# Kernel tuning notes

Measured on AMD Instinct MI355X. Metric: run time of the kernel, lower is better.

The kernel has to match this reference:

```python
import jax, jax.numpy as jnp
import numpy as np
import math

SEQ_LEN = 1024
NUM_FILTERS = 24
INPUT_DIM = 256
OUTPUT_DIM = 256
BATCH = 4


def _spectral_filters(seq_len, K):
    # Hankel matrix Z[i,j] = 2 / ((i+j)^3 - (i+j)), i,j in 1..L (use_hankel_L=False)
    entries = np.arange(1, seq_len + 1, dtype=np.float64)
    ipj = entries[:, None] + entries[None, :]
    Z = 2.0 / (ipj ** 3 - ipj)
    sigma, phi = np.linalg.eigh(Z)
    phi_k = phi[:, -K:] * (sigma[-K:] ** 0.25)
    return jnp.asarray(phi_k, dtype=jnp.float32)  # [L, K]


def setup_inputs() -> dict:
    key = jax.random.key(0)
    k1, k2, k3 = jax.random.split(key, 3)
    scale = (NUM_FILTERS * INPUT_DIM) ** (-0.5)
    x = jax.random.normal(k1, (BATCH, SEQ_LEN, INPUT_DIM), dtype=jnp.float32)
    phi = _spectral_filters(SEQ_LEN, NUM_FILTERS)
    M_phi_plus = jax.random.normal(k2, (NUM_FILTERS, INPUT_DIM, OUTPUT_DIM), dtype=jnp.float32) * scale
    M_phi_minus = jax.random.normal(k3, (NUM_FILTERS, INPUT_DIM, OUTPUT_DIM), dtype=jnp.float32) * scale
    return {"x": x, "phi": phi, "M_phi_plus": M_phi_plus, "M_phi_minus": M_phi_minus}


def reference(x, phi, M_phi_plus, M_phi_minus):
    B, L, I = x.shape
    n = 1 << math.ceil(math.log2(2 * L - 1))  # FFT length (2048 for L=1024)
    # alternating sign: +1 at even positions, -1 at odd (sgn[:,1::2] *= -1)
    sgn = jnp.where(jnp.arange(L) % 2 == 1, -1.0, 1.0).astype(jnp.float32)
    # FFT of filters: [F, K]
    V = jnp.fft.rfft(phi.astype(jnp.float32), n=n, axis=0)
    # FFT of input and sign-modulated input: [B, F, I]
    X = jnp.fft.rfft(x, n=n, axis=1)
    Xs = jnp.fft.rfft(x * sgn[None, :, None], n=n, axis=1)
    # pointwise multiply in frequency, broadcast over K: [B, F, K, I]
    U_plus = jnp.fft.irfft(V[None, :, :, None] * X[:, :, None, :], n=n, axis=1)[:, :L]
    U_minus = jnp.fft.irfft(V[None, :, :, None] * Xs[:, :, None, :], n=n, axis=1)[:, :L]
    U_minus = U_minus * sgn[None, :, None, None]
    # spectral projection: [B, L, O]
    out = jnp.einsum('blki,kio->blo', U_plus, M_phi_plus)
    out = out + jnp.einsum('blki,kio->blo', U_minus, M_phi_minus)
    return out
```

## Files before the change

### kernel.cpp

```cpp
#include <hip/hip_runtime.h>


#define ZB_ 12582912

typedef __attribute__((ext_vector_type(8))) short bf16x8;
typedef __attribute__((ext_vector_type(4))) float f32x4;

__device__ inline unsigned short f2bf(float f) {
    unsigned u = __float_as_uint(f);
    u += 0x7FFFu + ((u >> 16) & 1u);
    return (unsigned short)(u >> 16);
}

__device__ inline void gl16(const unsigned short* g, unsigned short* l) {
    __builtin_amdgcn_global_load_lds((const __attribute__((address_space(1))) void*)g,
                                     (__attribute__((address_space(3))) void*)l, 16, 0, 0);
}

__global__ __launch_bounds__(256) void k_prep_all(const float* __restrict__ x,
                                                  const float* __restrict__ phi,
                                                  const float* __restrict__ Mp,
                                                  const float* __restrict__ Mm,
                                                  unsigned short* __restrict__ xb,
                                                  unsigned short* __restrict__ ToepA,
                                                  unsigned short* __restrict__ MbT) {
    __shared__ float tile[32][33];
    int bid = blockIdx.x, tid = threadIdx.x;
    if (bid < 1024) {
        int i = (bid * 256 + tid) * 4;
        float4 v = *(const float4*)(x + i);
        ushort4 o;
        o.x = f2bf(v.x); o.y = f2bf(v.y); o.z = f2bf(v.z); o.w = f2bf(v.w);
        int row = i >> 8, col = i & 255;
        int dst = (row << 8) | (col & 192) | ((col & 63) ^ ((row & 7) << 3));
        *(ushort4*)(xb + dst) = o;
    } else if (bid < 1792) {
        int r = bid - 1024;
        int kk = r >> 4;
        int dm = (r & 15) - 1;
        int k = (kk < 24) ? kk : kk - 24;
        int i = tid >> 1, j0 = (tid & 1) * 32;
        unsigned short* dst = ToepA + ((size_t)kk * 16 + (dm + 1)) * 8192 + i * 64;
        int sw = (i & 7) << 3;
#pragma unroll
        for (int q = 0; q < 8; ++q) {
            int j = j0 + q * 4;
            unsigned short e[4];
#pragma unroll
            for (int ee = 0; ee < 4; ++ee) {
                int t = dm * 64 + i - (j + ee);
                float v = 0.f;
                if (t >= 0 && t < 1024) {
                    v = phi[t * 24 + k];
                    if (kk >= 24 && (t & 1)) v = -v;
                }
                e[ee] = f2bf(v);
            }
            ushort4 ov; ov.x = e[0]; ov.y = e[1]; ov.z = e[2]; ov.w = e[3];
            *(ushort4*)(dst + (j ^ sw)) = ov;
        }
    } else {
        int flat = bid - 1792;
        int kk = flat >> 6, rr = flat & 63;
        int i0 = (rr >> 3) * 32, o0 = (rr & 7) * 32;
        int tx = tid & 31, ty = tid >> 5;
        const float* src = ((kk < 24) ? Mp : Mm) + (size_t)((kk < 24) ? kk : kk - 24) * 65536;
        for (int j = 0; j < 4; ++j)
            tile[ty + j * 8][tx] = src[(i0 + ty + j * 8) * 256 + o0 + tx];
        __syncthreads();
        for (int j = 0; j < 4; ++j) {
            int orow = o0 + ty + j * 8, i = i0 + tx;
            int ic = (i & 192) | ((i & 63) ^ ((orow & 7) << 3));
            MbT[(size_t)kk * 65536 + orow * 256 + ic] = f2bf(tile[tx][ty + j * 8]);
        }
    }
}

__global__ __launch_bounds__(256, 2) void k_stage1(const unsigned short* __restrict__ xb0,
                                                   const unsigned short* __restrict__ MbT,
                                                   unsigned short* __restrict__ Z) {
    __shared__ unsigned short Ab[2][8192];
    __shared__ unsigned short Bb[3][8192];
    int tid = threadIdx.x, lane = tid & 63, w = tid >> 6;
    int wm = w >> 1, wn = w & 1;
    int m0 = blockIdx.x * 128;
    int kk = blockIdx.y >> 1;
    int o0 = (blockIdx.y & 1) * 128;
    int b  = blockIdx.z;
    const unsigned short* xb_b = xb0 + (size_t)b * 262144;
    unsigned short* Zb = Z + (size_t)b * ZB_;
    const unsigned short* Bsrc = MbT + (size_t)kk * 65536;
    int l16 = lane & 15, kofs = (lane >> 4) * 8;
    int sw = (l16 & 7) << 3;
    int r8 = lane >> 3, cg = lane & 7;

    int arow[4], brow[4], lofs[4];
#pragma unroll
    for (int q = 0; q < 4; ++q) {
        int rr = q * 32 + w * 8 + r8;
        arow[q] = (m0 + rr) * 256 + cg * 8;
        brow[q] = (o0 + rr) * 256 + cg * 8;
        lofs[q] = q * 2048 + w * 512;
    }

    f32x4 acc[4][4];
    for (int i = 0; i < 4; ++i)
        for (int j = 0; j < 4; ++j) {
            acc[i][j][0] = 0.f; acc[i][j][1] = 0.f; acc[i][j][2] = 0.f; acc[i][j][3] = 0.f;
        }

    auto stageA = [&](int bi, int ko) {
#pragma unroll
        for (int q = 0; q < 4; ++q) gl16(xb_b + arow[q] + ko * 64, &Ab[bi][0] + lofs[q]);
    };
    auto stageB = [&](int bi, int ko) {
#pragma unroll
        for (int q = 0; q < 4; ++q) gl16(Bsrc + brow[q] + ko * 64, &Bb[bi][0] + lofs[q]);
    };

    stageA(0, 0); stageB(0, 0); stageB(1, 1);

    for (int ko = 0; ko < 4; ++ko) {
        if (ko < 3) { asm volatile("s_waitcnt vmcnt(4)" ::: "memory"); }
        else        { asm volatile("s_waitcnt vmcnt(0)" ::: "memory"); }
        __builtin_amdgcn_sched_barrier(0);
        __builtin_amdgcn_s_barrier();
        __builtin_amdgcn_sched_barrier(0);
        if (ko < 3) stageA((ko + 1) & 1, ko + 1);
        if (ko < 2) stageB((ko + 2) % 3, ko + 2);

        const unsigned short* Abase = &Ab[ko & 1][0];
        const unsigned short* Bbase = &Bb[ko % 3][0];
        __builtin_amdgcn_s_setprio(1);
#pragma unroll
        for (int ks = 0; ks < 2; ++ks) {
            int koX = (ks * 32 + kofs) ^ sw;
            bf16x8 af[4], bfv[4];
#pragma unroll
            for (int mi = 0; mi < 4; ++mi)
                af[mi] = *(const bf16x8*)(Abase + (wm * 64 + mi * 16 + l16) * 64 + koX);
#pragma unroll
            for (int ni = 0; ni < 4; ++ni)
                bfv[ni] = *(const bf16x8*)(Bbase + (wn * 64 + ni * 16 + l16) * 64 + koX);
#pragma unroll
            for (int mi = 0; mi < 4; ++mi)
#pragma unroll
                for (int ni = 0; ni < 4; ++ni)
                    acc[mi][ni] = __builtin_amdgcn_mfma_f32_16x16x32_bf16(af[mi], bfv[ni], acc[mi][ni], 0, 0, 0);
        }
        __builtin_amdgcn_s_setprio(0);
    }

    int r4 = (lane >> 4) * 4;
    for (int mi = 0; mi < 4; ++mi) {
        int sbase = m0 + wm * 64 + mi * 16 + r4;
        for (int ni = 0; ni < 4; ++ni) {
            int o = o0 + wn * 64 + ni * 16 + l16;
            ushort4 pk;
            pk.x = f2bf(acc[mi][ni][0]); pk.y = f2bf(acc[mi][ni][1]);
            pk.z = f2bf(acc[mi][ni][2]); pk.w = f2bf(acc[mi][ni][3]);
            *(ushort4*)(Zb + (size_t)kk * 262144 + (size_t)o * 1024 + (sbase ^ ((o & 7) << 3))) = pk;
        }
    }
}

__global__ __launch_bounds__(256, 2) void k_stage2(const unsigned short* __restrict__ Z,
                                                   const unsigned short* __restrict__ ToepA,
                                                   float* __restrict__ partial, int kkpg) {
    __shared__ unsigned short Abuf[2][8192];
    __shared__ unsigned short Zbuf[3][8192];
    int tid = threadIdx.x, lane = tid & 63, w = tid >> 6;
    int wm = w >> 1, wn = w & 1;

    int gy = gridDim.y, nwg = 4 * gy * gridDim.z;
    int orig = blockIdx.x + blockIdx.y * 4 + blockIdx.z * 4 * gy;
    int wg = (orig & 7) * (nwg >> 3) + (orig >> 3);
    int pr = wg & 3;
    int yy = (wg >> 2) % gy;
    int zz = (wg >> 2) / gy;
    int o0 = (yy & 1) * 128;
    int b  = yy >> 1;
    int kgi = zz;
    int kk0 = kgi * kkpg;

    int l16 = lane & 15, kofs = (lane >> 4) * 8;
    int sw = (l16 & 7) << 3;
    int r8 = lane >> 3, cg = lane & 7;

    const unsigned short* Zb = Z + (size_t)b * ZB_;
    float* pb = partial + ((size_t)b * gridDim.z + kgi) * 262144;

    int arow[4], zrow[4], lofs[4];
#pragma unroll
    for (int q = 0; q < 4; ++q) {
        int rr = q * 32 + w * 8 + r8;
        arow[q] = rr * 64 + cg * 8;
        zrow[q] = (o0 + rr) * 1024 + cg * 8;
        lofs[q] = q * 2048 + w * 512;
    }

    for (int half = 0; half < 2; ++half) {
        int lb = half ? (7 - pr) : pr;
        int l0 = lb * 128;
        int nch = 2 * lb + 2;
        int total = kkpg * nch;

        f32x4 acc[4][4];
        for (int i = 0; i < 4; ++i)
            for (int j = 0; j < 4; ++j) {
                acc[i][j][0] = 0.f; acc[i][j][1] = 0.f; acc[i][j][2] = 0.f; acc[i][j][3] = 0.f;
            }

        __syncthreads();

        auto stageA = [&](int bi, int kka, int didx) {
            const unsigned short* gA = ToepA + ((size_t)kka * 16 + didx) * 8192;
#pragma unroll
            for (int q = 0; q < 4; ++q) gl16(gA + arow[q], &Abuf[bi][0] + lofs[q]);
        };
        auto stageZ = [&](int bi, int kka, int s0) {
            const unsigned short* gZ = Zb + (size_t)kka * 262144 + s0;
#pragma unroll
            for (int q = 0; q < 4; ++q) gl16(gZ + zrow[q], &Zbuf[bi][0] + lofs[q]);
        };
        auto compute = [&](int ba, int bz) {
            const unsigned short* Abase = &Abuf[ba][0];
            const unsigned short* Zbase = &Zbuf[bz][0];
            __builtin_amdgcn_s_setprio(1);
#pragma unroll
            for (int ks = 0; ks < 2; ++ks) {
                int koX = (ks * 32 + kofs) ^ sw;
                bf16x8 af[4], bfv[4];
#pragma unroll
                for (int mi = 0; mi < 4; ++mi)
                    af[mi] = *(const bf16x8*)(Abase + (wm * 64 + mi * 16 + l16) * 64 + koX);
#pragma unroll
                for (int ni = 0; ni < 4; ++ni)
                    bfv[ni] = *(const bf16x8*)(Zbase + (wn * 64 + ni * 16 + l16) * 64 + koX);
#pragma unroll
                for (int mi = 0; mi < 4; ++mi)
#pragma unroll
                    for (int ni = 0; ni < 4; ++ni)
                        acc[mi][ni] = __builtin_amdgcn_mfma_f32_16x16x32_bf16(af[mi], bfv[ni], acc[mi][ni], 0, 0, 0);
            }
            __builtin_amdgcn_s_setprio(0);
        };

        stageA(0, kk0, 2 * lb + 1);
        stageZ(0, kk0, 0);
        stageZ(1, kk0, 64);

        int scA = 1, kkA = 0;
        int scZ = 2, kkZ = 0;
        if (scZ == nch) { scZ = 0; kkZ = 1; }
        int jz = 2;

        for (int j = 0; j < total - 1; ++j) {
            asm volatile("s_waitcnt vmcnt(4)" ::: "memory");
            __builtin_amdgcn_sched_barrier(0);
            __builtin_amdgcn_s_barrier();
            __builtin_amdgcn_sched_barrier(0);
            stageA((j + 1) & 1, kk0 + kkA, 2 * lb - scA + 1);
            ++scA; if (scA == nch) { scA = 0; ++kkA; }
            if (jz < total) {
                stageZ(jz % 3, kk0 + kkZ, scZ * 64);
                ++scZ; if (scZ == nch) { scZ = 0; ++kkZ; }
                ++jz;
            }
            compute(j & 1, j % 3);
        }
        asm volatile("s_waitcnt vmcnt(0)" ::: "memory");
        __builtin_amdgcn_sched_barrier(0);
        __builtin_amdgcn_s_barrier();
        __builtin_amdgcn_sched_barrier(0);
        compute((total - 1) & 1, (total - 1) % 3);

        int r4 = (lane >> 4) * 4;
        for (int mi = 0; mi < 4; ++mi) {
            int l = l0 + wm * 64 + mi * 16 + r4;
            for (int ni = 0; ni < 4; ++ni) {
                int o = o0 + wn * 64 + ni * 16 + l16;
                float* dst = pb + (size_t)l * 256 + o;
                dst[0]   = acc[mi][ni][0];
                dst[256] = acc[mi][ni][1];
                dst[512] = acc[mi][ni][2];
                dst[768] = acc[mi][ni][3];
            }
        }
    }
}

__global__ void k_reduce(const float* __restrict__ partial, float* __restrict__ outg, int kg) {
    const float* pb = partial + (size_t)blockIdx.y * kg * 262144;
    int i = (blockIdx.x * 256 + threadIdx.x) * 4;
    float4 s = *(const float4*)(pb + i);
    for (int kgi = 1; kgi < kg; ++kgi) {
        float4 v = *(const float4*)(pb + (size_t)kgi * 262144 + i);
        s.x += v.x; s.y += v.y; s.z += v.z; s.w += v.w;
    }
    *(float4*)(outg + (size_t)blockIdx.y * 262144 + i) = s;
}

extern "C" void kernel_launch(void* const* d_in, const int* in_sizes, int n_in,
                              void* d_out, int out_size, void* d_ws, size_t ws_size,
                              hipStream_t stream) {
    const float* x   = (const float*)d_in[0];
    const float* phi = (const float*)d_in[1];
    const float* Mp  = (const float*)d_in[2];
    const float* Mm  = (const float*)d_in[3];
    float* out = (float*)d_out;

    char* ws = (char*)d_ws;
    unsigned short* xb    = (unsigned short*)(ws);
    unsigned short* MbT   = (unsigned short*)(ws + 2097152);
    unsigned short* ToepA = (unsigned short*)(ws + 8388608);
    unsigned short* Zbuf  = (unsigned short*)(ws + 20971520);
    const size_t fixed = 20971520;

    int g = 4, kg = 16;
    auto need = [&](int gg, int kk) {
        return fixed + (size_t)gg * 25165824 + (size_t)gg * (size_t)kk * 1048576;
    };
    if (need(4, 16) > ws_size) {
        kg = 12;
        if (need(4, 12) > ws_size) {
            g = 2; kg = 16;
            if (need(2, 16) > ws_size) {
                kg = 12;
                if (need(2, 12) > ws_size) {
                    g = 1; kg = 16;
                    if (need(1, 16) > ws_size) {
                        kg = 12;
                        if (need(1, 12) > ws_size) kg = 6;
                    }
                }
            }
        }
    }
    float* partial = (float*)(ws + fixed + (size_t)g * 25165824);

    k_prep_all<<<dim3(4864), dim3(256), 0, stream>>>(x, phi, Mp, Mm, xb, ToepA, MbT);

    for (int b0 = 0; b0 < 4; b0 += g) {
        k_stage1<<<dim3(8, 96, g), dim3(256), 0, stream>>>(xb + (size_t)b0 * 262144, MbT, Zbuf);
        k_stage2<<<dim3(4, 2 * g, kg), dim3(256), 0, stream>>>(Zbuf, ToepA, partial, 48 / kg);
        k_reduce<<<dim3(256, g), dim3(256), 0, stream>>>(partial, out + (size_t)b0 * 262144, kg);
    }
}
```

Measured before the change: 147.7 us.

## Shrink stage1 k-tile, raise occupancy, remap blocks, and store bf16 partials

Stage1 now stages 32-wide K slices instead of 64, halving LDS per block so launch bounds can allow four blocks per CU, and the swizzle of xb and MbT changes to match the 32-wide rows. Stage1 also remaps block indices so neighbouring blocks are spread across XCDs. Stage2 writes its partial sums as bf16 instead of fp32, and the reduce kernel reads bf16 eight values at a time and sums them in fp32. This halves partial-buffer traffic but adds extra rounding error to partial sums before reduction, and stage1 runs more K iterations with more barriers.

```diff
diff --git a/kernel.cpp b/kernel.cpp
--- a/kernel.cpp
+++ b/kernel.cpp
@@ -10,6 +10,11 @@
     unsigned u = __float_as_uint(f);
     u += 0x7FFFu + ((u >> 16) & 1u);
     return (unsigned short)(u >> 16);
+}
+
+__device__ inline float bf2f(unsigned short s) {
+    unsigned u = ((unsigned)s) << 16;
+    return __uint_as_float(u);
 }
 
 __device__ inline void gl16(const unsigned short* g, unsigned short* l) {
@@ -32,7 +37,7 @@
         ushort4 o;
         o.x = f2bf(v.x); o.y = f2bf(v.y); o.z = f2bf(v.z); o.w = f2bf(v.w);
         int row = i >> 8, col = i & 255;
-        int dst = (row << 8) | (col & 192) | ((col & 63) ^ ((row & 7) << 3));
+        int dst = (row << 8) | (col & 224) | ((col & 31) ^ (((row >> 1) & 3) << 3));
         *(ushort4*)(xb + dst) = o;
     } else if (bid < 1792) {
         int r = bid - 1024;
@@ -70,36 +75,43 @@
         __syncthreads();
         for (int j = 0; j < 4; ++j) {
             int orow = o0 + ty + j * 8, i = i0 + tx;
-            int ic = (i & 192) | ((i & 63) ^ ((orow & 7) << 3));
+            int ic = (i & 224) | ((i & 31) ^ (((orow >> 1) & 3) << 3));
             MbT[(size_t)kk * 65536 + orow * 256 + ic] = f2bf(tile[tx][ty + j * 8]);
         }
     }
 }
 
-__global__ __launch_bounds__(256, 2) void k_stage1(const unsigned short* __restrict__ xb0,
+__global__ __launch_bounds__(256, 4) void k_stage1(const unsigned short* __restrict__ xb0,
                                                    const unsigned short* __restrict__ MbT,
                                                    unsigned short* __restrict__ Z) {
-    __shared__ unsigned short Ab[2][8192];
-    __shared__ unsigned short Bb[3][8192];
+    __shared__ unsigned short Ab[2][4096];
+    __shared__ unsigned short Bb[3][4096];
     int tid = threadIdx.x, lane = tid & 63, w = tid >> 6;
     int wm = w >> 1, wn = w & 1;
-    int m0 = blockIdx.x * 128;
-    int kk = blockIdx.y >> 1;
-    int o0 = (blockIdx.y & 1) * 128;
-    int b  = blockIdx.z;
+
+    int nwg = 768 * gridDim.z;
+    int orig = blockIdx.x + blockIdx.y * 8 + blockIdx.z * 768;
+    int wg = (orig & 7) * (nwg >> 3) + (orig >> 3);
+    int m0 = (wg & 7) * 128;
+    int rem = wg >> 3;
+    int yy = rem % 96;
+    int b  = rem / 96;
+    int kk = yy >> 1;
+    int o0 = (yy & 1) * 128;
+
     const unsigned short* xb_b = xb0 + (size_t)b * 262144;
     unsigned short* Zb = Z + (size_t)b * ZB_;
     const unsigned short* Bsrc = MbT + (size_t)kk * 65536;
     int l16 = lane & 15, kofs = (lane >> 4) * 8;
-    int sw = (l16 & 7) << 3;
-    int r8 = lane >> 3, cg = lane & 7;
-
-    int arow[4], brow[4], lofs[4];
-#pragma unroll
-    for (int q = 0; q < 4; ++q) {
-        int rr = q * 32 + w * 8 + r8;
-        arow[q] = (m0 + rr) * 256 + cg * 8;
-        brow[q] = (o0 + rr) * 256 + cg * 8;
+    int sw32 = ((l16 >> 1) & 3) << 3;
+    int r4l = lane >> 2, c4 = (lane & 3) * 8;
+
+    int arow[2], brow[2], lofs[2];
+#pragma unroll
+    for (int q = 0; q < 2; ++q) {
+        int rr = q * 64 + w * 16 + r4l;
+        arow[q] = (m0 + rr) * 256 + c4;
+        brow[q] = (o0 + rr) * 256 + c4;
         lofs[q] = q * 2048 + w * 512;
     }
 
@@ -111,43 +123,40 @@
 
     auto stageA = [&](int bi, int ko) {
 #pragma unroll
-        for (int q = 0; q < 4; ++q) gl16(xb_b + arow[q] + ko * 64, &Ab[bi][0] + lofs[q]);
+        for (int q = 0; q < 2; ++q) gl16(xb_b + arow[q] + ko * 32, &Ab[bi][0] + lofs[q]);
     };
     auto stageB = [&](int bi, int ko) {
 #pragma unroll
-        for (int q = 0; q < 4; ++q) gl16(Bsrc + brow[q] + ko * 64, &Bb[bi][0] + lofs[q]);
+        for (int q = 0; q < 2; ++q) gl16(Bsrc + brow[q] + ko * 32, &Bb[bi][0] + lofs[q]);
     };
 
     stageA(0, 0); stageB(0, 0); stageB(1, 1);
 
-    for (int ko = 0; ko < 4; ++ko) {
-        if (ko < 3) { asm volatile("s_waitcnt vmcnt(4)" ::: "memory"); }
+    for (int ko = 0; ko < 8; ++ko) {
+        if (ko < 7) { asm volatile("s_waitcnt vmcnt(2)" ::: "memory"); }
         else        { asm volatile("s_waitcnt vmcnt(0)" ::: "memory"); }
         __builtin_amdgcn_sched_barrier(0);
         __builtin_amdgcn_s_barrier();
         __builtin_amdgcn_sched_barrier(0);
-        if (ko < 3) stageA((ko + 1) & 1, ko + 1);
-        if (ko < 2) stageB((ko + 2) % 3, ko + 2);
+        if (ko < 7) stageA((ko + 1) & 1, ko + 1);
+        if (ko < 6) stageB((ko + 2) % 3, ko + 2);
 
         const unsigned short* Abase = &Ab[ko & 1][0];
         const unsigned short* Bbase = &Bb[ko % 3][0];
+        int koX = kofs ^ sw32;
+        bf16x8 af[4], bfv[4];
+#pragma unroll
+        for (int mi = 0; mi < 4; ++mi)
+            af[mi] = *(const bf16x8*)(Abase + (wm * 64 + mi * 16 + l16) * 32 + koX);
+#pragma unroll
+        for (int ni = 0; ni < 4; ++ni)
+            bfv[ni] = *(const bf16x8*)(Bbase + (wn * 64 + ni * 16 + l16) * 32 + koX);
         __builtin_amdgcn_s_setprio(1);
 #pragma unroll
-        for (int ks = 0; ks < 2; ++ks) {
-            int koX = (ks * 32 + kofs) ^ sw;
-            bf16x8 af[4], bfv[4];
-#pragma unroll
-            for (int mi = 0; mi < 4; ++mi)
-                af[mi] = *(const bf16x8*)(Abase + (wm * 64 + mi * 16 + l16) * 64 + koX);
+        for (int mi = 0; mi < 4; ++mi)
 #pragma unroll
             for (int ni = 0; ni < 4; ++ni)
-                bfv[ni] = *(const bf16x8*)(Bbase + (wn * 64 + ni * 16 + l16) * 64 + koX);
-#pragma unroll
-            for (int mi = 0; mi < 4; ++mi)
-#pragma unroll
-                for (int ni = 0; ni < 4; ++ni)
-                    acc[mi][ni] = __builtin_amdgcn_mfma_f32_16x16x32_bf16(af[mi], bfv[ni], acc[mi][ni], 0, 0, 0);
-        }
+                acc[mi][ni] = __builtin_amdgcn_mfma_f32_16x16x32_bf16(af[mi], bfv[ni], acc[mi][ni], 0, 0, 0);
         __builtin_amdgcn_s_setprio(0);
     }
 
@@ -166,7 +175,7 @@
 
 __global__ __launch_bounds__(256, 2) void k_stage2(const unsigned short* __restrict__ Z,
                                                    const unsigned short* __restrict__ ToepA,
-                                                   float* __restrict__ partial, int kkpg) {
+                                                   unsigned short* __restrict__ partial, int kkpg) {
     __shared__ unsigned short Abuf[2][8192];
     __shared__ unsigned short Zbuf[3][8192];
     int tid = threadIdx.x, lane = tid & 63, w = tid >> 6;
@@ -188,7 +197,7 @@
     int r8 = lane >> 3, cg = lane & 7;
 
     const unsigned short* Zb = Z + (size_t)b * ZB_;
-    float* pb = partial + ((size_t)b * gridDim.z + kgi) * 262144;
+    unsigned short* pb = partial + ((size_t)b * gridDim.z + kgi) * 262144;
 
     int arow[4], zrow[4], lofs[4];
 #pragma unroll
@@ -280,25 +289,37 @@
             int l = l0 + wm * 64 + mi * 16 + r4;
             for (int ni = 0; ni < 4; ++ni) {
                 int o = o0 + wn * 64 + ni * 16 + l16;
-                float* dst = pb + (size_t)l * 256 + o;
-                dst[0]   = acc[mi][ni][0];
-                dst[256] = acc[mi][ni][1];
-                dst[512] = acc[mi][ni][2];
-                dst[768] = acc[mi][ni][3];
-            }
-        }
-    }
-}
-
-__global__ void k_reduce(const float* __restrict__ partial, float* __restrict__ outg, int kg) {
-    const float* pb = partial + (size_t)blockIdx.y * kg * 262144;
-    int i = (blockIdx.x * 256 + threadIdx.x) * 4;
-    float4 s = *(const float4*)(pb + i);
-    for (int kgi = 1; kgi < kg; ++kgi) {
-        float4 v = *(const float4*)(pb + (size_t)kgi * 262144 + i);
-        s.x += v.x; s.y += v.y; s.z += v.z; s.w += v.w;
-    }
-    *(float4*)(outg + (size_t)blockIdx.y * 262144 + i) = s;
+                unsigned short* dst = pb + (size_t)l * 256 + o;
+                dst[0]   = f2bf(acc[mi][ni][0]);
+                dst[256] = f2bf(acc[mi][ni][1]);
+                dst[512] = f2bf(acc[mi][ni][2]);
+                dst[768] = f2bf(acc[mi][ni][3]);
+            }
+        }
+    }
+}
+
+__global__ void k_reduce(const unsigned short* __restrict__ partial, float* __restrict__ outg, int kg) {
+    const unsigned short* pb = partial + (size_t)blockIdx.y * kg * 262144;
+    int i = (blockIdx.x * 256 + threadIdx.x) * 8;
+    float s[8];
+#pragma unroll
+    for (int j = 0; j < 8; ++j) s[j] = 0.f;
+    for (int kgi = 0; kgi < kg; ++kgi) {
+        uint4 v = *(const uint4*)(pb + (size_t)kgi * 262144 + i);
+        unsigned vv[4] = {v.x, v.y, v.z, v.w};
+#pragma unroll
+        for (int q = 0; q < 4; ++q) {
+            s[q * 2]     += bf2f((unsigned short)(vv[q] & 0xFFFF));
+            s[q * 2 + 1] += bf2f((unsigned short)(vv[q] >> 16));
+        }
+    }
+    float4 o0, o1;
+    o0.x = s[0]; o0.y = s[1]; o0.z = s[2]; o0.w = s[3];
+    o1.x = s[4]; o1.y = s[5]; o1.z = s[6]; o1.w = s[7];
+    float* dst = outg + (size_t)blockIdx.y * 262144 + i;
+    *(float4*)(dst) = o0;
+    *(float4*)(dst + 4) = o1;
 }
 
 extern "C" void kernel_launch(void* const* d_in, const int* in_sizes, int n_in,
@@ -319,7 +340,7 @@
 
     int g = 4, kg = 16;
     auto need = [&](int gg, int kk) {
-        return fixed + (size_t)gg * 25165824 + (size_t)gg * (size_t)kk * 1048576;
+        return fixed + (size_t)gg * 25165824 + (size_t)gg * (size_t)kk * 524288;
     };
     if (need(4, 16) > ws_size) {
         kg = 12;
@@ -337,13 +358,13 @@
             }
         }
     }
-    float* partial = (float*)(ws + fixed + (size_t)g * 25165824);
+    unsigned short* partial = (unsigned short*)(ws + fixed + (size_t)g * 25165824);
 
     k_prep_all<<<dim3(4864), dim3(256), 0, stream>>>(x, phi, Mp, Mm, xb, ToepA, MbT);
 
     for (int b0 = 0; b0 < 4; b0 += g) {
         k_stage1<<<dim3(8, 96, g), dim3(256), 0, stream>>>(xb + (size_t)b0 * 262144, MbT, Zbuf);
         k_stage2<<<dim3(4, 2 * g, kg), dim3(256), 0, stream>>>(Zbuf, ToepA, partial, 48 / kg);
-        k_reduce<<<dim3(256, g), dim3(256), 0, stream>>>(partial, out + (size_t)b0 * 262144, kg);
-    }
-}
+        k_reduce<<<dim3(128, g), dim3(256), 0, stream>>>(partial, out + (size_t)b0 * 262144, kg);
+    }
+}
```

Result: faster. 130.7 us, median of 3 (-11.5%).
